# Performance work log

Measured on AMD Instinct MI355X. Metric: run time of the kernel, lower is better.

## Reference

```python
import jax, jax.numpy as jnp
import numpy as np

EPS = 1e-5

def _inst_norm(x):
    # x: (B,C,H,W); torch .var(dim=2) is unbiased (ddof=1) over HW
    B, C, H, W = x.shape
    xf = x.reshape(B, C, H * W)
    mean = xf.mean(axis=2, keepdims=True)
    var = xf.var(axis=2, ddof=1, keepdims=True) + EPS
    return ((xf - mean) / jnp.sqrt(var)).reshape(B, C, H, W)

def _conv1x1(x, w, b):
    # (out,in) weight applied channelwise
    return jnp.einsum('oc,bchw->bohw', w, x) + b[None, :, None, None]

def setup_inputs() -> dict:
    key = jax.random.key(0)
    ks = jax.random.split(key, 10)
    B, C, H, W = 4, 512, 64, 64
    s = 1.0 / np.sqrt(C)
    return {
        'x_fcc': jax.random.normal(ks[0], (B, C, H, W), jnp.float32),
        'x_fss': jax.random.normal(ks[1], (B, C, H, W), jnp.float32),
        'w1': jax.random.normal(ks[2], (C, C), jnp.float32) * s,
        'b1': jax.random.normal(ks[3], (C,), jnp.float32) * 0.01,
        'w2': jax.random.normal(ks[4], (C, C), jnp.float32) * s,
        'b2': jax.random.normal(ks[5], (C,), jnp.float32) * 0.01,
        'w3': jax.random.normal(ks[6], (C, C), jnp.float32) * s,
        'b3': jax.random.normal(ks[7], (C,), jnp.float32) * 0.01,
        'wrs': jax.random.normal(ks[8], (C, C), jnp.float32) * s,
        'brs': jax.random.normal(ks[9], (C,), jnp.float32) * 0.01,
    }

def reference(x_fcc, x_fss, w1, b1, w2, b2, w3, b3, wrs, brs):
    Bc, Cc, Hc, Wc = x_fcc.shape
    Bs, Cs, Hs, Ws = x_fss.shape
    q = _conv1x1(_inst_norm(x_fcc), w1, b1).reshape(Bc, Cc, Hc * Wc)
    k = _conv1x1(_inst_norm(x_fss), w2, b2).reshape(Bs, Cs, Hs * Ws)
    v = _conv1x1(x_fss, w3, b3).reshape(Bc, Cs, Hs * Ws)
    # attention: (B, HWc, HWs), softmax over style positions
    scores = jnp.einsum('bcq,bck->bqk', q, k)
    A = jax.nn.softmax(scores, axis=-1)
    # aggregate style values per content position: (B, C, HWc)
    frs = jnp.einsum('bck,bqk->bcq', v, A).reshape(x_fcc.shape)
    frs = _conv1x1(frs, wrs, brs)
    return frs + x_fcc
```

## Files before the change

### kernel.cpp

```cpp
#include <hip/hip_runtime.h>
#include <hip/hip_bf16.h>


typedef _Float16 f16_t;
typedef _Float16 f16x8 __attribute__((ext_vector_type(8)));
typedef float f32x4 __attribute__((ext_vector_type(4)));

#define C_DIM 512
#define HW_DIM 4096
#define NBATCH 4
#define CHW (512L * 4096L)

__device__ inline f32x4 mfma_f16(f16x8 a, f16x8 b, f32x4 c) {
    return __builtin_amdgcn_mfma_f32_16x16x32_f16(a, b, c, 0, 0, 0);
}

__device__ inline void g2l16(const f16_t* g, f16_t* l) {
    auto gp = (const __attribute__((address_space(1))) uint32_t*)(uintptr_t)g;
    auto lp = (__attribute__((address_space(3))) uint32_t*)(uint32_t)(uintptr_t)l;
    __builtin_amdgcn_global_load_lds(gp, lp, 16, 0, 0);
}

template<int N> __device__ inline void vmwait() {
    static_assert(N == 0 || N == 3 || N == 4 || N == 6, "add vmcnt case");
    if constexpr (N == 0)      asm volatile("s_waitcnt vmcnt(0)" ::: "memory");
    else if constexpr (N == 3) asm volatile("s_waitcnt vmcnt(3)" ::: "memory");
    else if constexpr (N == 4) asm volatile("s_waitcnt vmcnt(4)" ::: "memory");
    else                       asm volatile("s_waitcnt vmcnt(6)" ::: "memory");
}

__global__ __launch_bounds__(256) void stats_kernel(
    const float* __restrict__ xc, const float* __restrict__ xs,
    float* __restrict__ meanc, float* __restrict__ rstdc,
    float* __restrict__ means, float* __restrict__ rstds)
{
    int id = blockIdx.x;
    int bc = id & 2047;
    const float4* x = (const float4*)((id < 2048 ? xc : xs) + (size_t)bc * HW_DIM);
    int tid = threadIdx.x;
    float s = 0.f, ss = 0.f;
#pragma unroll
    for (int i = 0; i < 4; i++) {
        float4 v = x[tid + (i << 8)];
        s += v.x + v.y + v.z + v.w;
        ss += v.x * v.x + v.y * v.y + v.z * v.z + v.w * v.w;
    }
#pragma unroll
    for (int o = 32; o; o >>= 1) { s += __shfl_down(s, o); ss += __shfl_down(ss, o); }
    __shared__ float red[8];
    if ((tid & 63) == 0) { red[(tid >> 6) * 2] = s; red[(tid >> 6) * 2 + 1] = ss; }
    __syncthreads();
    if (tid == 0) {
        s  = red[0] + red[2] + red[4] + red[6];
        ss = red[1] + red[3] + red[5] + red[7];
        float mean = s * (1.0f / 4096.0f);
        float var  = (ss - 4096.0f * mean * mean) * (1.0f / 4095.0f);
        float rstd = rsqrtf(var + 1e-5f);
        if (id < 2048) { meanc[bc] = mean; rstdc[bc] = rstd; }
        else           { means[bc] = mean; rstds[bc] = rstd; }
    }
}

__global__ __launch_bounds__(256) void pack_w4_kernel(
    const float* __restrict__ w0, const float* __restrict__ w1,
    const float* __restrict__ w2, const float* __restrict__ w3,
    f16_t* __restrict__ h0, f16_t* __restrict__ h1,
    f16_t* __restrict__ h2, f16_t* __restrict__ h3,
    const float* __restrict__ bb0, const float* __restrict__ bb1,
    const float* __restrict__ bb2, const float* __restrict__ bb3,
    float* __restrict__ biasws)
{
    int which = blockIdx.y;
    const float* w = which == 0 ? w0 : which == 1 ? w1 : which == 2 ? w2 : w3;
    f16_t* h = which == 0 ? h0 : which == 1 ? h1 : which == 2 ? h2 : h3;
    const float* bs = which == 0 ? bb0 : which == 1 ? bb1 : which == 2 ? bb2 : bb3;
    int i = blockIdx.x * 256 + threadIdx.x;
    h[i] = (f16_t)w[i];
    if (i < C_DIM) biasws[which * C_DIM + i] = bs[i];
}

__global__ __launch_bounds__(256) void pack_T_kernel(
    const float* __restrict__ xc, const float* __restrict__ xs,
    const float* __restrict__ meanc, const float* __restrict__ rstdc,
    const float* __restrict__ means, const float* __restrict__ rstds,
    f16_t* __restrict__ ch, f16_t* __restrict__ sh, f16_t* __restrict__ sraw)
{
    __shared__ float tile[32][33];
    int z = blockIdx.z;
    int b = z & 3, src = z >> 2;
    const float* x    = (src == 0) ? xc : xs;
    const float* mean = (src == 0) ? meanc : means;
    const float* rstd = (src == 0) ? rstdc : rstds;
    f16_t* oh = (src == 0) ? ch : (src == 1) ? sh : sraw;
    bool norm = (src < 2);

    int c0 = blockIdx.y * 32, p0 = blockIdx.x * 32;
    int tp = threadIdx.x & 31, tc8 = threadIdx.x >> 5;
    const float* xb = x + ((size_t)b * C_DIM + c0) * HW_DIM + p0;
#pragma unroll
    for (int it = 0; it < 4; it++) {
        int c = tc8 + it * 8;
        float v = xb[(size_t)c * HW_DIM + tp];
        if (norm) {
            float m = mean[b * C_DIM + c0 + c];
            float r = rstd[b * C_DIM + c0 + c];
            v = (v - m) * r;
        }
        tile[c][tp] = v;
    }
    __syncthreads();
    int wc = threadIdx.x & 31, wp8 = threadIdx.x >> 5;
    f16_t* ohb = oh + ((size_t)b * HW_DIM + p0) * C_DIM + c0;
#pragma unroll
    for (int it = 0; it < 4; it++) {
        int p = wp8 + it * 8;
        ohb[(size_t)p * C_DIM + wc] = (f16_t)tile[wc][p];
    }
}

__global__ __launch_bounds__(256) void softmax_rows(
    const float* __restrict__ S, f16_t* __restrict__ P)
{
    int row = blockIdx.x;
    int tid = threadIdx.x;
    int wave = tid >> 6, lane = tid & 63;
    const float4* sr = (const float4*)(S + (size_t)row * HW_DIM);
    float4 v[4];
    float mx = -3.4e38f;
#pragma unroll
    for (int i = 0; i < 4; i++) {
        v[i] = sr[tid + (i << 8)];
        mx = fmaxf(mx, fmaxf(fmaxf(v[i].x, v[i].y), fmaxf(v[i].z, v[i].w)));
    }
#pragma unroll
    for (int o = 32; o; o >>= 1) mx = fmaxf(mx, __shfl_down(mx, o));
    __shared__ float red[4];
    if (lane == 0) red[wave] = mx;
    __syncthreads();
    mx = fmaxf(fmaxf(red[0], red[1]), fmaxf(red[2], red[3]));
    float sum = 0.f;
#pragma unroll
    for (int i = 0; i < 4; i++) {
        v[i].x = __expf(v[i].x - mx); v[i].y = __expf(v[i].y - mx);
        v[i].z = __expf(v[i].z - mx); v[i].w = __expf(v[i].w - mx);
        sum += v[i].x + v[i].y + v[i].z + v[i].w;
    }
#pragma unroll
    for (int o = 32; o; o >>= 1) sum += __shfl_down(sum, o);
    __syncthreads();
    if (lane == 0) red[wave] = sum;
    __syncthreads();
    sum = red[0] + red[1] + red[2] + red[3];
    float inv = 1.0f / sum;
    uint2* pr = (uint2*)(P + (size_t)row * HW_DIM);
#pragma unroll
    for (int i = 0; i < 4; i++) {
        union { uint2 u; f16_t h[4]; } o;
        o.h[0] = (f16_t)(v[i].x * inv); o.h[1] = (f16_t)(v[i].y * inv);
        o.h[2] = (f16_t)(v[i].z * inv); o.h[3] = (f16_t)(v[i].w * inv);
        pr[tid + (i << 8)] = o.u;
    }
}

__global__ __launch_bounds__(256) void reduce4_kernel(
    const float* __restrict__ part, f16_t* __restrict__ out)
{
    size_t i = (size_t)blockIdx.x * 256 + threadIdx.x;
    const float4* p0 = (const float4*)part;
    const float4* p1 = (const float4*)(part + CHW);
    const float4* p2 = (const float4*)(part + 2 * CHW);
    const float4* p3 = (const float4*)(part + 3 * CHW);
    float4 a = p0[i], b = p1[i], c = p2[i], d = p3[i];
    union { uint2 u; f16_t h[4]; } o;
    o.h[0] = (f16_t)(a.x + b.x + c.x + d.x);
    o.h[1] = (f16_t)(a.y + b.y + c.y + d.y);
    o.h[2] = (f16_t)(a.z + b.z + c.z + d.z);
    o.h[3] = (f16_t)(a.w + b.w + c.w + d.w);
    ((uint2*)out)[i] = o.u;
}

template<int WM, int WN, int EPI, bool QK, int KT, int CHX, int CHY>
__global__ __launch_bounds__(256) void gemm_nt(
    const f16_t* __restrict__ Ah, const f16_t* __restrict__ Bh,
    void* __restrict__ Cout0,
    const float* __restrict__ bias, const float* __restrict__ resid,
    int lda, int ldc,
    long sAz, long sBz, long sCz, long sRz, long sAw, long sBw, long sCw)
{
    constexpr int BM = 2 * WM * 16;
    constexpr int BN = 2 * WN * 16;
    constexpr int BK = 32;
    constexpr int NIT = KT / BK;
    constexpr int BUFSZ = (BM + BN) * BK;
    constexpr int AOPS = BM / 64;
    constexpr int BOPS = BN / 64;
    constexpr int OPS  = AOPS + BOPS;
    __shared__ __align__(16) f16_t smem[3 * BUFSZ];

    int bx, by, bz;
    if constexpr (CHX > 0) {
        const int nbx = gridDim.x, nby = gridDim.y, nbz = gridDim.z;
        const int lin = (blockIdx.z * nby + blockIdx.y) * nbx + blockIdx.x;
        const int nwg = nbx * nby * nbz;
        const int cpx = nwg >> 3;
        const int logical = (lin & 7) * cpx + (lin >> 3);
        constexpr int CHB = CHX * CHY;
        const int chunk  = logical / CHB;
        const int within = logical % CHB;
        const int cx = within % CHX, cy = within / CHX;
        const int chunks_x = nbx / CHX;
        const int chx = chunk % chunks_x;
        int t = chunk / chunks_x;
        const int chunks_y = nby / CHY;
        const int chy = t % chunks_y;
        bz = t / chunks_y;
        bx = chx * CHX + cx;
        by = chy * CHY + cy;
    } else {
        bx = blockIdx.x; by = blockIdx.y; bz = blockIdx.z;
    }

    const int tid  = threadIdx.x;
    const int wave = tid >> 6, lane = tid & 63;
    const int wm = (wave >> 1) * (WM * 16);
    const int wn = (wave & 1) * (WN * 16);
    const int fr = lane & 15;
    const int fk = (lane >> 4) * 8;
    const int srow = lane >> 2;
    const int scol = (lane & 3) * 8;

    const long mBlock = (long)by * BM;
    const long nBlock = (long)bx * BN;
    const int zz = bz;
    const int z   = QK ? (zz & 3) : zz;
    const int sel = QK ? (zz >> 2) : 0;
    const f16_t* Az = Ah + (size_t)z * sAz + (size_t)sel * sAw;
    const f16_t* Bz = Bh + (size_t)z * sBz + (size_t)sel * sBw;
    const float* biasp = bias ? (bias + (QK ? sel * C_DIM : 0)) : nullptr;

    const f16_t* gA = Az + (size_t)(mBlock + srow) * lda + scol;
    const f16_t* gB = Bz + (size_t)(nBlock + srow) * lda + scol;

    const f16_t* srcA[AOPS]; int dstA[AOPS];
    const f16_t* srcB[BOPS]; int dstB[BOPS];
#pragma unroll
    for (int i = 0; i < AOPS; i++) {
        int seg = i * 4 + wave;
        srcA[i] = gA + (size_t)seg * 16 * lda;
        dstA[i] = seg * 512;
    }
#pragma unroll
    for (int i = 0; i < BOPS; i++) {
        int seg = i * 4 + wave;
        srcB[i] = gB + (size_t)seg * 16 * lda;
        dstB[i] = BM * BK + seg * 512;
    }

    auto stage = [&](int t) {
        f16_t* dst = smem + (t % 3) * BUFSZ;
        const int k0 = t * BK;
#pragma unroll
        for (int i = 0; i < AOPS; i++) g2l16(srcA[i] + k0, dst + dstA[i]);
#pragma unroll
        for (int i = 0; i < BOPS; i++) g2l16(srcB[i] + k0, dst + dstB[i]);
    };

    f32x4 acc[WM][WN];
#pragma unroll
    for (int i = 0; i < WM; i++)
#pragma unroll
        for (int j = 0; j < WN; j++)
            acc[i][j] = (f32x4){0.f, 0.f, 0.f, 0.f};

    stage(0);
    stage(1);
    vmwait<OPS>();
    __builtin_amdgcn_s_barrier();
    __builtin_amdgcn_sched_barrier(0);

#pragma unroll
    for (int t = 0; t < NIT; ++t) {
        if (t + 2 < NIT) {
            stage(t + 2);
            __builtin_amdgcn_sched_barrier(0);
        }
        const f16_t* sA = smem + (t % 3) * BUFSZ;
        const f16_t* sB = sA + BM * BK;
        f16x8 af[WM], bf[WN];
#pragma unroll
        for (int i = 0; i < WM; i++)
            af[i] = *reinterpret_cast<const f16x8*>(sA + (wm + i * 16 + fr) * BK + fk);
#pragma unroll
        for (int j = 0; j < WN; j++)
            bf[j] = *reinterpret_cast<const f16x8*>(sB + (wn + j * 16 + fr) * BK + fk);
        __builtin_amdgcn_s_setprio(1);
#pragma unroll
        for (int i = 0; i < WM; i++)
#pragma unroll
            for (int j = 0; j < WN; j++)
                acc[i][j] = mfma_f16(af[i], bf[j], acc[i][j]);
        __builtin_amdgcn_s_setprio(0);

        if (t + 2 < NIT)      vmwait<OPS>();
        else if (t + 1 < NIT) vmwait<0>();
        if (t + 1 < NIT) {
            __builtin_amdgcn_s_barrier();
            __builtin_amdgcn_sched_barrier(0);
        }
    }

    const int col  = lane & 15;
    const int rowq = (lane >> 4) * 4;
    const size_t cbase = (size_t)z * sCz + (size_t)sel * sCw;
#pragma unroll
    for (int i = 0; i < WM; i++) {
        const long mb = mBlock + wm + i * 16 + rowq;
        float bv[4];
#pragma unroll
        for (int r = 0; r < 4; r++) bv[r] = biasp ? biasp[mb + r] : 0.0f;
#pragma unroll
        for (int j = 0; j < WN; j++) {
            const long n = nBlock + wn + j * 16 + col;
            float v[4];
#pragma unroll
            for (int r = 0; r < 4; r++) v[r] = acc[i][j][r] + bv[r];
            if constexpr (EPI == 0) {
                float* O = (float*)Cout0 + cbase;
                const float* R = resid ? (resid + (size_t)z * sRz) : nullptr;
#pragma unroll
                for (int r = 0; r < 4; r++) {
                    size_t off = (size_t)(mb + r) * ldc + n;
                    O[off] = v[r] + (R ? R[off] : 0.0f);
                }
            } else if constexpr (EPI == 1) {
                f16_t* O = (f16_t*)Cout0 + cbase;
#pragma unroll
                for (int r = 0; r < 4; r++) O[(size_t)(mb + r) * ldc + n] = (f16_t)v[r];
            } else if constexpr (EPI == 3) {
                alignas(8) f16_t h[4];
#pragma unroll
                for (int r = 0; r < 4; r++) h[r] = (f16_t)v[r];
                size_t offo = cbase + (size_t)n * ldc + mb;
                *reinterpret_cast<uint2*>((f16_t*)Cout0 + offo) = *reinterpret_cast<uint2*>(h);
            } else {
                alignas(16) float h[4];
#pragma unroll
                for (int r = 0; r < 4; r++) h[r] = v[r];
                size_t offo = cbase + (size_t)n * ldc + mb;
                *reinterpret_cast<float4*>((float*)Cout0 + offo) = *reinterpret_cast<float4*>(h);
            }
        }
    }
}

extern "C" void kernel_launch(void* const* d_in, const int* in_sizes, int n_in,
                              void* d_out, int out_size, void* d_ws, size_t ws_size,
                              hipStream_t stream)
{
    const float* x_fcc = (const float*)d_in[0];
    const float* x_fss = (const float*)d_in[1];
    const float* w1 = (const float*)d_in[2];
    const float* b1 = (const float*)d_in[3];
    const float* w2 = (const float*)d_in[4];
    const float* b2 = (const float*)d_in[5];
    const float* w3 = (const float*)d_in[6];
    const float* b3 = (const float*)d_in[7];
    const float* wrs = (const float*)d_in[8];
    const float* brs = (const float*)d_in[9];
    float* out = (float*)d_out;
    (void)n_in; (void)in_sizes; (void)out_size; (void)ws_size;

    char* base = (char*)d_ws;
    size_t off = 0;
    auto take = [&](size_t bytes) -> char* {
        char* p = base + off;
        off += (bytes + 255) & ~(size_t)255;
        return p;
    };
    const size_t WB = (size_t)C_DIM * C_DIM * sizeof(f16_t);
    const size_t TB = (size_t)NBATCH * CHW * sizeof(f16_t);
    const long  TBe = NBATCH * CHW;

    float* meanc = (float*)take(2048 * 4);
    float* rstdc = (float*)take(2048 * 4);
    float* means = (float*)take(2048 * 4);
    float* rstds = (float*)take(2048 * 4);
    float* biasws = (float*)take(4 * C_DIM * 4);
    f16_t* w1h = (f16_t*)take(WB);
    f16_t* w2h = (f16_t*)take(WB);
    f16_t* w3h = (f16_t*)take(WB);
    f16_t* wrh = (f16_t*)take(WB);
    f16_t* qT = (f16_t*)take(TB);
    f16_t* kT = (f16_t*)take(TB);
    f16_t* vh   = (f16_t*)take(TB);
    f16_t* frsT = (f16_t*)take(TB);
    char* packb = take(8 * TB);
    f16_t* xcT  = (f16_t*)(packb);
    f16_t* xsT  = (f16_t*)(packb + TB);
    f16_t* xsrT = (f16_t*)(packb + 2 * TB);
    float* Smat = (float*)(packb);
    f16_t* Pmat = (f16_t*)(packb + 4 * TB);
    float* Part = (float*)(packb + 6 * TB);

    dim3 blk(256);

    stats_kernel<<<dim3(4096), blk, 0, stream>>>(x_fcc, x_fss, meanc, rstdc, means, rstds);
    pack_w4_kernel<<<dim3(1024, 4), blk, 0, stream>>>(
        w1, w2, w3, wrs, w1h, w2h, w3h, wrh, b1, b2, b3, brs, biasws);
    pack_T_kernel<<<dim3(128, 16, 12), blk, 0, stream>>>(
        x_fcc, x_fss, meanc, rstdc, means, rstds, xcT, xsT, xsrT);
    gemm_nt<4, 4, 3, true, C_DIM, 16, 4><<<dim3(32, 4, 8), blk, 0, stream>>>(
        w1h, xcT, qT, biasws, nullptr, C_DIM, C_DIM,
        0L, CHW, CHW, 0L, (long)C_DIM * C_DIM, TBe, TBe);
    gemm_nt<4, 4, 1, false, C_DIM, 16, 4><<<dim3(32, 4, 4), blk, 0, stream>>>(
        w3h, xsrT, vh, biasws + 2 * C_DIM, nullptr, C_DIM, HW_DIM,
        0L, CHW, CHW, 0L, 0L, 0L, 0L);
    for (int b = 0; b < NBATCH; b++) {
        gemm_nt<4, 4, 0, false, C_DIM, 8, 8><<<dim3(32, 32, 1), blk, 0, stream>>>(
            qT + (size_t)b * CHW, kT + (size_t)b * CHW,
            Smat, nullptr, nullptr, C_DIM, HW_DIM,
            0L, 0L, 0L, 0L, 0L, 0L, 0L);
        softmax_rows<<<dim3(4096), blk, 0, stream>>>(Smat, Pmat);
        gemm_nt<2, 4, 4, false, 1024, 8, 8><<<dim3(32, 8, 4), blk, 0, stream>>>(
            vh + (size_t)b * CHW, Pmat,
            Part, nullptr, nullptr, HW_DIM, C_DIM,
            1024L, 1024L, CHW, 0L, 0L, 0L, 0L);
        reduce4_kernel<<<dim3(CHW / 1024), blk, 0, stream>>>(
            Part, frsT + (size_t)b * CHW);
    }
    gemm_nt<4, 4, 0, false, C_DIM, 16, 4><<<dim3(32, 4, 4), blk, 0, stream>>>(
        wrh, frsT, out, biasws + 3 * C_DIM, x_fcc, C_DIM, HW_DIM,
        0L, CHW, CHW, CHW, 0L, 0L, 0L);
}
```

Baseline: 599.3 us.

## Add 256x128 swizzled-LDS GEMM kernel for QK, scores and PV with split-K 8

```diff
diff --git a/kernel.cpp b/kernel.cpp
--- a/kernel.cpp
+++ b/kernel.cpp
@@ -27,6 +27,11 @@
     else if constexpr (N == 3) asm volatile("s_waitcnt vmcnt(3)" ::: "memory");
     else if constexpr (N == 4) asm volatile("s_waitcnt vmcnt(4)" ::: "memory");
     else                       asm volatile("s_waitcnt vmcnt(6)" ::: "memory");
+}
+
+__device__ inline void barrier_mem() {
+    asm volatile("s_barrier" ::: "memory");
+    __builtin_amdgcn_sched_barrier(0);
 }
 
 __global__ __launch_bounds__(256) void stats_kernel(
@@ -162,21 +167,177 @@
     }
 }
 
-__global__ __launch_bounds__(256) void reduce4_kernel(
+__global__ __launch_bounds__(256) void reduce8_kernel(
     const float* __restrict__ part, f16_t* __restrict__ out)
 {
     size_t i = (size_t)blockIdx.x * 256 + threadIdx.x;
-    const float4* p0 = (const float4*)part;
-    const float4* p1 = (const float4*)(part + CHW);
-    const float4* p2 = (const float4*)(part + 2 * CHW);
-    const float4* p3 = (const float4*)(part + 3 * CHW);
-    float4 a = p0[i], b = p1[i], c = p2[i], d = p3[i];
+    float4 s = ((const float4*)part)[i];
+#pragma unroll
+    for (int p = 1; p < 8; p++) {
+        float4 v = ((const float4*)(part + (size_t)p * CHW))[i];
+        s.x += v.x; s.y += v.y; s.z += v.z; s.w += v.w;
+    }
     union { uint2 u; f16_t h[4]; } o;
-    o.h[0] = (f16_t)(a.x + b.x + c.x + d.x);
-    o.h[1] = (f16_t)(a.y + b.y + c.y + d.y);
-    o.h[2] = (f16_t)(a.z + b.z + c.z + d.z);
-    o.h[3] = (f16_t)(a.w + b.w + c.w + d.w);
+    o.h[0] = (f16_t)s.x; o.h[1] = (f16_t)s.y;
+    o.h[2] = (f16_t)s.z; o.h[3] = (f16_t)s.w;
     ((uint2*)out)[i] = o.u;
+}
+
+template<int EPI, bool QK, int CHX, int CHY>
+__global__ __launch_bounds__(512, 2) void gemm256(
+    const f16_t* __restrict__ Ah, const f16_t* __restrict__ Bh,
+    void* __restrict__ Cout0, const float* __restrict__ bias,
+    int lda, int ldc,
+    long sAz, long sBz, long sCz, long sAw, long sBw, long sCw)
+{
+    constexpr int NT = 8;
+    constexpr int AE = 256 * 64;
+    constexpr int BE = 128 * 64;
+    constexpr int BUFE = AE + BE;
+    __shared__ __align__(16) f16_t smem[3 * BUFE];
+
+    int bx, by, bz;
+    {
+        const int nbx = gridDim.x, nby = gridDim.y, nbz = gridDim.z;
+        const int lin = ((int)blockIdx.z * nby + blockIdx.y) * nbx + blockIdx.x;
+        const int nwg = nbx * nby * nbz;
+        const int cpx = nwg >> 3;
+        const int logical = (lin & 7) * cpx + (lin >> 3);
+        constexpr int CHB = CHX * CHY;
+        const int chunk  = logical / CHB;
+        const int within = logical % CHB;
+        const int cx = within % CHX, cy = within / CHX;
+        const int chunks_x = nbx / CHX;
+        const int chx = chunk % chunks_x;
+        int tt = chunk / chunks_x;
+        const int chunks_y = nby / CHY;
+        bz = tt / chunks_y;
+        by = (tt % chunks_y) * CHY + cy;
+        bx = chx * CHX + cx;
+    }
+
+    const int tid  = threadIdx.x;
+    const int wave = tid >> 6, lane = tid & 63;
+    const int wm = (wave >> 2) * 128;
+    const int wn = (wave & 3) * 32;
+    const int fr = lane & 15;
+    const int g16 = lane >> 4;
+    const int key = fr & 7;
+
+    const int z   = QK ? (bz & 3) : bz;
+    const int sel = QK ? (bz >> 2) : 0;
+    const f16_t* Az = Ah + (size_t)z * sAz + (size_t)sel * sAw;
+    const f16_t* Bz = Bh + (size_t)z * sBz + (size_t)sel * sBw;
+    const float* biasp = bias ? (bias + (QK ? sel * C_DIM : 0)) : nullptr;
+    const long mBlock = (long)by * 256;
+    const long nBlock = (long)bx * 128;
+
+    const int srow8 = lane >> 3;
+    const int gsrc  = ((lane & 7) ^ srow8) * 8;
+    const f16_t* aSrc[4]; const f16_t* bSrc[2];
+    int aDst[4], bDst[2];
+#pragma unroll
+    for (int q = 0; q < 4; q++) {
+        int j = 4 * wave + q;
+        aSrc[q] = Az + (size_t)(mBlock + 8 * j + srow8) * lda + gsrc;
+        aDst[q] = j * 512;
+    }
+#pragma unroll
+    for (int q = 0; q < 2; q++) {
+        int j = 2 * wave + q;
+        bSrc[q] = Bz + (size_t)(nBlock + 8 * j + srow8) * lda + gsrc;
+        bDst[q] = AE + j * 512;
+    }
+
+    auto stageA = [&](int t) {
+        f16_t* dst = smem + (t % 3) * BUFE;
+        const int k0 = t * 64;
+#pragma unroll
+        for (int q = 0; q < 4; q++) g2l16(aSrc[q] + k0, dst + aDst[q]);
+    };
+    auto stageB = [&](int t) {
+        f16_t* dst = smem + (t % 3) * BUFE;
+        const int k0 = t * 64;
+#pragma unroll
+        for (int q = 0; q < 2; q++) g2l16(bSrc[q] + k0, dst + bDst[q]);
+    };
+
+    f32x4 acc[8][2];
+#pragma unroll
+    for (int i = 0; i < 8; i++)
+#pragma unroll
+        for (int j = 0; j < 2; j++) acc[i][j] = (f32x4){0.f, 0.f, 0.f, 0.f};
+
+    stageA(0); stageB(0); stageA(1); stageB(1);
+    vmwait<6>();
+    barrier_mem();
+
+#pragma unroll
+    for (int t = 0; t < NT; ++t) {
+        const f16_t* buf = smem + (t % 3) * BUFE;
+#pragma unroll
+        for (int ks = 0; ks < 2; ++ks) {
+            f16x8 a[8], b[2];
+            const int gr = ((ks * 4 + g16) ^ key) * 8;
+#pragma unroll
+            for (int j2 = 0; j2 < 2; j2++)
+                b[j2] = *reinterpret_cast<const f16x8*>(
+                    buf + AE + (wn + j2 * 16 + fr) * 64 + gr);
+#pragma unroll
+            for (int mi = 0; mi < 8; mi++)
+                a[mi] = *reinterpret_cast<const f16x8*>(
+                    buf + (wm + mi * 16 + fr) * 64 + gr);
+            if (t + 2 < NT) { if (ks == 0) stageA(t + 2); else stageB(t + 2); }
+            if (ks == 1) {
+                if (t + 2 < NT)      vmwait<6>();
+                else if (t + 1 < NT) vmwait<0>();
+            }
+            barrier_mem();
+            __builtin_amdgcn_s_setprio(1);
+#pragma unroll
+            for (int mi = 0; mi < 8; mi++)
+#pragma unroll
+                for (int j2 = 0; j2 < 2; j2++)
+                    acc[mi][j2] = mfma_f16(a[mi], b[j2], acc[mi][j2]);
+            __builtin_amdgcn_s_setprio(0);
+            barrier_mem();
+        }
+    }
+
+    const int col  = lane & 15;
+    const int rowq = (lane >> 4) * 4;
+    const size_t cbase = (size_t)z * sCz + (size_t)sel * sCw;
+#pragma unroll
+    for (int mi = 0; mi < 8; mi++) {
+        const long mb = mBlock + wm + mi * 16 + rowq;
+        float bv[4];
+#pragma unroll
+        for (int r = 0; r < 4; r++) bv[r] = biasp ? biasp[mb + r] : 0.0f;
+#pragma unroll
+        for (int j2 = 0; j2 < 2; j2++) {
+            const long n = nBlock + wn + j2 * 16 + col;
+            float v[4];
+#pragma unroll
+            for (int r = 0; r < 4; r++) v[r] = acc[mi][j2][r] + bv[r];
+            if constexpr (EPI == 0) {
+                float* O = (float*)Cout0 + cbase;
+#pragma unroll
+                for (int r = 0; r < 4; r++) O[(size_t)(mb + r) * ldc + n] = v[r];
+            } else if constexpr (EPI == 3) {
+                alignas(8) f16_t h[4];
+#pragma unroll
+                for (int r = 0; r < 4; r++) h[r] = (f16_t)v[r];
+                *reinterpret_cast<uint2*>((f16_t*)Cout0 + cbase + (size_t)n * ldc + mb)
+                    = *reinterpret_cast<uint2*>(h);
+            } else {
+                alignas(16) float h[4];
+#pragma unroll
+                for (int r = 0; r < 4; r++) h[r] = v[r];
+                *reinterpret_cast<float4*>((float*)Cout0 + cbase + (size_t)n * ldc + mb)
+                    = *reinterpret_cast<float4*>(h);
+            }
+        }
+    }
 }
 
 template<int WM, int WN, int EPI, bool QK, int KT, int CHX, int CHY>
@@ -280,10 +441,7 @@
 
 #pragma unroll
     for (int t = 0; t < NIT; ++t) {
-        if (t + 2 < NIT) {
-            stage(t + 2);
-            __builtin_amdgcn_sched_barrier(0);
-        }
+        if (t + 2 < NIT) stage(t + 2);
         const f16_t* sA = smem + (t % 3) * BUFSZ;
         const f16_t* sB = sA + BM * BK;
         f16x8 af[WM], bf[WN];
@@ -293,13 +451,11 @@
 #pragma unroll
         for (int j = 0; j < WN; j++)
             bf[j] = *reinterpret_cast<const f16x8*>(sB + (wn + j * 16 + fr) * BK + fk);
-        __builtin_amdgcn_s_setprio(1);
 #pragma unroll
         for (int i = 0; i < WM; i++)
 #pragma unroll
             for (int j = 0; j < WN; j++)
                 acc[i][j] = mfma_f16(af[i], bf[j], acc[i][j]);
-        __builtin_amdgcn_s_setprio(0);
 
         if (t + 2 < NIT)      vmwait<OPS>();
         else if (t + 1 < NIT) vmwait<0>();
@@ -400,32 +556,33 @@
     f16_t* xsrT = (f16_t*)(packb + 2 * TB);
     float* Smat = (float*)(packb);
     f16_t* Pmat = (f16_t*)(packb + 4 * TB);
-    float* Part = (float*)(packb + 6 * TB);
+    float* Part = (float*)(packb);
 
     dim3 blk(256);
+    dim3 blk5(512);
 
     stats_kernel<<<dim3(4096), blk, 0, stream>>>(x_fcc, x_fss, meanc, rstdc, means, rstds);
     pack_w4_kernel<<<dim3(1024, 4), blk, 0, stream>>>(
         w1, w2, w3, wrs, w1h, w2h, w3h, wrh, b1, b2, b3, brs, biasws);
     pack_T_kernel<<<dim3(128, 16, 12), blk, 0, stream>>>(
         x_fcc, x_fss, meanc, rstdc, means, rstds, xcT, xsT, xsrT);
-    gemm_nt<4, 4, 3, true, C_DIM, 16, 4><<<dim3(32, 4, 8), blk, 0, stream>>>(
-        w1h, xcT, qT, biasws, nullptr, C_DIM, C_DIM,
-        0L, CHW, CHW, 0L, (long)C_DIM * C_DIM, TBe, TBe);
+    gemm256<3, true, 8, 2><<<dim3(32, 2, 8), blk5, 0, stream>>>(
+        w1h, xcT, qT, biasws, C_DIM, C_DIM,
+        0L, CHW, CHW, (long)C_DIM * C_DIM, TBe, TBe);
     gemm_nt<4, 4, 1, false, C_DIM, 16, 4><<<dim3(32, 4, 4), blk, 0, stream>>>(
         w3h, xsrT, vh, biasws + 2 * C_DIM, nullptr, C_DIM, HW_DIM,
         0L, CHW, CHW, 0L, 0L, 0L, 0L);
     for (int b = 0; b < NBATCH; b++) {
-        gemm_nt<4, 4, 0, false, C_DIM, 8, 8><<<dim3(32, 32, 1), blk, 0, stream>>>(
+        gemm256<0, false, 8, 4><<<dim3(32, 16, 1), blk5, 0, stream>>>(
             qT + (size_t)b * CHW, kT + (size_t)b * CHW,
-            Smat, nullptr, nullptr, C_DIM, HW_DIM,
-            0L, 0L, 0L, 0L, 0L, 0L, 0L);
+            Smat, nullptr, C_DIM, HW_DIM,
+            0L, 0L, 0L, 0L, 0L, 0L);
         softmax_rows<<<dim3(4096), blk, 0, stream>>>(Smat, Pmat);
-        gemm_nt<2, 4, 4, false, 1024, 8, 8><<<dim3(32, 8, 4), blk, 0, stream>>>(
+        gemm256<4, false, 8, 2><<<dim3(32, 2, 8), blk5, 0, stream>>>(
             vh + (size_t)b * CHW, Pmat,
-            Part, nullptr, nullptr, HW_DIM, C_DIM,
-            1024L, 1024L, CHW, 0L, 0L, 0L, 0L);
-        reduce4_kernel<<<dim3(CHW / 1024), blk, 0, stream>>>(
+            Part, nullptr, HW_DIM, C_DIM,
+            512L, 512L, (long)CHW, 0L, 0L, 0L);
+        reduce8_kernel<<<dim3(CHW / 1024), blk, 0, stream>>>(
             Part, frsT + (size_t)b * CHW);
     }
     gemm_nt<4, 4, 0, false, C_DIM, 16, 4><<<dim3(32, 4, 4), blk, 0, stream>>>(
```

New measurement: 557.9 us. 6.9% less time.

## Replace GEMM with 256x128 tiled 512-thread kernel using swizzled LDS and BK=64

Applied to the files above, without the earlier changes.

```diff
diff --git a/kernel.cpp b/kernel.cpp
--- a/kernel.cpp
+++ b/kernel.cpp
@@ -22,11 +22,14 @@
 }
 
 template<int N> __device__ inline void vmwait() {
-    static_assert(N == 0 || N == 3 || N == 4 || N == 6, "add vmcnt case");
-    if constexpr (N == 0)      asm volatile("s_waitcnt vmcnt(0)" ::: "memory");
-    else if constexpr (N == 3) asm volatile("s_waitcnt vmcnt(3)" ::: "memory");
-    else if constexpr (N == 4) asm volatile("s_waitcnt vmcnt(4)" ::: "memory");
-    else                       asm volatile("s_waitcnt vmcnt(6)" ::: "memory");
+    static_assert(N == 0 || N == 6, "add vmcnt case");
+    if constexpr (N == 0) asm volatile("s_waitcnt vmcnt(0)" ::: "memory");
+    else                  asm volatile("s_waitcnt vmcnt(6)" ::: "memory");
+}
+
+__device__ inline void barrier_mem() {
+    asm volatile("s_barrier" ::: "memory");
+    __builtin_amdgcn_sched_barrier(0);
 }
 
 __global__ __launch_bounds__(256) void stats_kernel(
@@ -91,8 +94,6 @@
     const float* x    = (src == 0) ? xc : xs;
     const float* mean = (src == 0) ? meanc : means;
     const float* rstd = (src == 0) ? rstdc : rstds;
-    f16_t* oh = (src == 0) ? ch : (src == 1) ? sh : sraw;
-    bool norm = (src < 2);
 
     int c0 = blockIdx.y * 32, p0 = blockIdx.x * 32;
     int tp = threadIdx.x & 31, tc8 = threadIdx.x >> 5;
@@ -100,21 +101,21 @@
 #pragma unroll
     for (int it = 0; it < 4; it++) {
         int c = tc8 + it * 8;
-        float v = xb[(size_t)c * HW_DIM + tp];
-        if (norm) {
-            float m = mean[b * C_DIM + c0 + c];
-            float r = rstd[b * C_DIM + c0 + c];
-            v = (v - m) * r;
-        }
-        tile[c][tp] = v;
+        tile[c][tp] = xb[(size_t)c * HW_DIM + tp];
     }
     __syncthreads();
     int wc = threadIdx.x & 31, wp8 = threadIdx.x >> 5;
-    f16_t* ohb = oh + ((size_t)b * HW_DIM + p0) * C_DIM + c0;
+    float m = mean[b * C_DIM + c0 + wc];
+    float r = rstd[b * C_DIM + c0 + wc];
+    size_t obase = ((size_t)b * HW_DIM + p0) * C_DIM + c0;
+    f16_t* ohb = ((src == 0) ? ch : sh) + obase;
+    f16_t* srb = sraw + obase;
 #pragma unroll
     for (int it = 0; it < 4; it++) {
         int p = wp8 + it * 8;
-        ohb[(size_t)p * C_DIM + wc] = (f16_t)tile[wc][p];
+        float v = tile[wc][p];
+        ohb[(size_t)p * C_DIM + wc] = (f16_t)((v - m) * r);
+        if (src == 1) srb[(size_t)p * C_DIM + wc] = (f16_t)v;
     }
 }
 
@@ -179,28 +180,23 @@
     ((uint2*)out)[i] = o.u;
 }
 
-template<int WM, int WN, int EPI, bool QK, int KT, int CHX, int CHY>
-__global__ __launch_bounds__(256) void gemm_nt(
+template<int EPI, bool QK, int NT, int CHX, int CHY>
+__global__ __launch_bounds__(512, 2) void gemm256(
     const f16_t* __restrict__ Ah, const f16_t* __restrict__ Bh,
-    void* __restrict__ Cout0,
-    const float* __restrict__ bias, const float* __restrict__ resid,
+    void* __restrict__ Cout0, const float* __restrict__ bias,
+    const float* __restrict__ resid,
     int lda, int ldc,
     long sAz, long sBz, long sCz, long sRz, long sAw, long sBw, long sCw)
 {
-    constexpr int BM = 2 * WM * 16;
-    constexpr int BN = 2 * WN * 16;
-    constexpr int BK = 32;
-    constexpr int NIT = KT / BK;
-    constexpr int BUFSZ = (BM + BN) * BK;
-    constexpr int AOPS = BM / 64;
-    constexpr int BOPS = BN / 64;
-    constexpr int OPS  = AOPS + BOPS;
-    __shared__ __align__(16) f16_t smem[3 * BUFSZ];
+    constexpr int AE = 256 * 64;
+    constexpr int BE = 128 * 64;
+    constexpr int BUFE = AE + BE;
+    __shared__ __align__(16) f16_t smem[3 * BUFE];
 
     int bx, by, bz;
-    if constexpr (CHX > 0) {
+    {
         const int nbx = gridDim.x, nby = gridDim.y, nbz = gridDim.z;
-        const int lin = (blockIdx.z * nby + blockIdx.y) * nbx + blockIdx.x;
+        const int lin = ((int)blockIdx.z * nby + blockIdx.y) * nbx + blockIdx.x;
         const int nwg = nbx * nby * nbz;
         const int cpx = nwg >> 3;
         const int logical = (lin & 7) * cpx + (lin >> 3);
@@ -210,102 +206,98 @@
         const int cx = within % CHX, cy = within / CHX;
         const int chunks_x = nbx / CHX;
         const int chx = chunk % chunks_x;
-        int t = chunk / chunks_x;
+        int tt = chunk / chunks_x;
         const int chunks_y = nby / CHY;
-        const int chy = t % chunks_y;
-        bz = t / chunks_y;
+        bz = tt / chunks_y;
+        by = (tt % chunks_y) * CHY + cy;
         bx = chx * CHX + cx;
-        by = chy * CHY + cy;
-    } else {
-        bx = blockIdx.x; by = blockIdx.y; bz = blockIdx.z;
     }
 
     const int tid  = threadIdx.x;
     const int wave = tid >> 6, lane = tid & 63;
-    const int wm = (wave >> 1) * (WM * 16);
-    const int wn = (wave & 1) * (WN * 16);
+    const int wm = (wave >> 2) * 128;
+    const int wn = (wave & 3) * 32;
     const int fr = lane & 15;
-    const int fk = (lane >> 4) * 8;
-    const int srow = lane >> 2;
-    const int scol = (lane & 3) * 8;
-
-    const long mBlock = (long)by * BM;
-    const long nBlock = (long)bx * BN;
-    const int zz = bz;
-    const int z   = QK ? (zz & 3) : zz;
-    const int sel = QK ? (zz >> 2) : 0;
+    const int g16 = lane >> 4;
+    const int key = fr & 7;
+
+    const int z   = QK ? (bz & 3) : bz;
+    const int sel = QK ? (bz >> 2) : 0;
     const f16_t* Az = Ah + (size_t)z * sAz + (size_t)sel * sAw;
     const f16_t* Bz = Bh + (size_t)z * sBz + (size_t)sel * sBw;
     const float* biasp = bias ? (bias + (QK ? sel * C_DIM : 0)) : nullptr;
-
-    const f16_t* gA = Az + (size_t)(mBlock + srow) * lda + scol;
-    const f16_t* gB = Bz + (size_t)(nBlock + srow) * lda + scol;
-
-    const f16_t* srcA[AOPS]; int dstA[AOPS];
-    const f16_t* srcB[BOPS]; int dstB[BOPS];
-#pragma unroll
-    for (int i = 0; i < AOPS; i++) {
-        int seg = i * 4 + wave;
-        srcA[i] = gA + (size_t)seg * 16 * lda;
-        dstA[i] = seg * 512;
-    }
-#pragma unroll
-    for (int i = 0; i < BOPS; i++) {
-        int seg = i * 4 + wave;
-        srcB[i] = gB + (size_t)seg * 16 * lda;
-        dstB[i] = BM * BK + seg * 512;
-    }
-
-    auto stage = [&](int t) {
-        f16_t* dst = smem + (t % 3) * BUFSZ;
-        const int k0 = t * BK;
-#pragma unroll
-        for (int i = 0; i < AOPS; i++) g2l16(srcA[i] + k0, dst + dstA[i]);
-#pragma unroll
-        for (int i = 0; i < BOPS; i++) g2l16(srcB[i] + k0, dst + dstB[i]);
+    const long mBlock = (long)by * 256;
+    const long nBlock = (long)bx * 128;
+
+    const int srow8 = lane >> 3;
+    const int gsrc  = ((lane & 7) ^ srow8) * 8;
+    const f16_t* aSrc[4]; const f16_t* bSrc[2];
+    int aDst[4], bDst[2];
+#pragma unroll
+    for (int q = 0; q < 4; q++) {
+        int j = 4 * wave + q;
+        aSrc[q] = Az + (size_t)(mBlock + 8 * j + srow8) * lda + gsrc;
+        aDst[q] = j * 512;
+    }
+#pragma unroll
+    for (int q = 0; q < 2; q++) {
+        int j = 2 * wave + q;
+        bSrc[q] = Bz + (size_t)(nBlock + 8 * j + srow8) * lda + gsrc;
+        bDst[q] = AE + j * 512;
+    }
+
+    auto stageA = [&](int t) {
+        f16_t* dst = smem + (t % 3) * BUFE;
+        const int k0 = t * 64;
+#pragma unroll
+        for (int q = 0; q < 4; q++) g2l16(aSrc[q] + k0, dst + aDst[q]);
     };
-
-    f32x4 acc[WM][WN];
-#pragma unroll
-    for (int i = 0; i < WM; i++)
-#pragma unroll
-        for (int j = 0; j < WN; j++)
-            acc[i][j] = (f32x4){0.f, 0.f, 0.f, 0.f};
-
-    stage(0);
-    stage(1);
-    vmwait<OPS>();
-    __builtin_amdgcn_s_barrier();
-    __builtin_amdgcn_sched_barrier(0);
-
-#pragma unroll
-    for (int t = 0; t < NIT; ++t) {
-        if (t + 2 < NIT) {
-            stage(t + 2);
-            __builtin_amdgcn_sched_barrier(0);
-        }
-        const f16_t* sA = smem + (t % 3) * BUFSZ;
-        const f16_t* sB = sA + BM * BK;
-        f16x8 af[WM], bf[WN];
-#pragma unroll
-        for (int i = 0; i < WM; i++)
-            af[i] = *reinterpret_cast<const f16x8*>(sA + (wm + i * 16 + fr) * BK + fk);
-#pragma unroll
-        for (int j = 0; j < WN; j++)
-            bf[j] = *reinterpret_cast<const f16x8*>(sB + (wn + j * 16 + fr) * BK + fk);
-        __builtin_amdgcn_s_setprio(1);
-#pragma unroll
-        for (int i = 0; i < WM; i++)
-#pragma unroll
-            for (int j = 0; j < WN; j++)
-                acc[i][j] = mfma_f16(af[i], bf[j], acc[i][j]);
-        __builtin_amdgcn_s_setprio(0);
-
-        if (t + 2 < NIT)      vmwait<OPS>();
-        else if (t + 1 < NIT) vmwait<0>();
-        if (t + 1 < NIT) {
-            __builtin_amdgcn_s_barrier();
-            __builtin_amdgcn_sched_barrier(0);
+    auto stageB = [&](int t) {
+        f16_t* dst = smem + (t % 3) * BUFE;
+        const int k0 = t * 64;
+#pragma unroll
+        for (int q = 0; q < 2; q++) g2l16(bSrc[q] + k0, dst + bDst[q]);
+    };
+
+    f32x4 acc[8][2];
+#pragma unroll
+    for (int i = 0; i < 8; i++)
+#pragma unroll
+        for (int j = 0; j < 2; j++) acc[i][j] = (f32x4){0.f, 0.f, 0.f, 0.f};
+
+    stageA(0); stageB(0); stageA(1); stageB(1);
+    vmwait<6>();
+    barrier_mem();
+
+#pragma unroll
+    for (int t = 0; t < NT; ++t) {
+        const f16_t* buf = smem + (t % 3) * BUFE;
+#pragma unroll
+        for (int ks = 0; ks < 2; ++ks) {
+            f16x8 a[8], b[2];
+            const int gr = ((ks * 4 + g16) ^ key) * 8;
+#pragma unroll
+            for (int j2 = 0; j2 < 2; j2++)
+                b[j2] = *reinterpret_cast<const f16x8*>(
+                    buf + AE + (wn + j2 * 16 + fr) * 64 + gr);
+#pragma unroll
+            for (int mi = 0; mi < 8; mi++)
+                a[mi] = *reinterpret_cast<const f16x8*>(
+                    buf + (wm + mi * 16 + fr) * 64 + gr);
+            if (t + 2 < NT) { if (ks == 0) stageA(t + 2); else stageB(t + 2); }
+            if (ks == 1) {
+                if (t + 2 < NT)      vmwait<6>();
+                else if (t + 1 < NT) vmwait<0>();
+            }
+            barrier_mem();
+            __builtin_amdgcn_s_setprio(1);
+#pragma unroll
+            for (int mi = 0; mi < 8; mi++)
+#pragma unroll
+                for (int j2 = 0; j2 < 2; j2++)
+                    acc[mi][j2] = mfma_f16(a[mi], b[j2], acc[mi][j2]);
+            __builtin_amdgcn_s_setprio(0);
+            barrier_mem();
         }
     }
 
@@ -313,17 +305,17 @@
     const int rowq = (lane >> 4) * 4;
     const size_t cbase = (size_t)z * sCz + (size_t)sel * sCw;
 #pragma unroll
-    for (int i = 0; i < WM; i++) {
-        const long mb = mBlock + wm + i * 16 + rowq;
+    for (int mi = 0; mi < 8; mi++) {
+        const long mb = mBlock + wm + mi * 16 + rowq;
         float bv[4];
 #pragma unroll
         for (int r = 0; r < 4; r++) bv[r] = biasp ? biasp[mb + r] : 0.0f;
 #pragma unroll
-        for (int j = 0; j < WN; j++) {
-            const long n = nBlock + wn + j * 16 + col;
+        for (int j2 = 0; j2 < 2; j2++) {
+            const long n = nBlock + wn + j2 * 16 + col;
             float v[4];
 #pragma unroll
-            for (int r = 0; r < 4; r++) v[r] = acc[i][j][r] + bv[r];
+            for (int r = 0; r < 4; r++) v[r] = acc[mi][j2][r] + bv[r];
             if constexpr (EPI == 0) {
                 float* O = (float*)Cout0 + cbase;
                 const float* R = resid ? (resid + (size_t)z * sRz) : nullptr;
@@ -340,14 +332,14 @@
                 alignas(8) f16_t h[4];
 #pragma unroll
                 for (int r = 0; r < 4; r++) h[r] = (f16_t)v[r];
-                size_t offo = cbase + (size_t)n * ldc + mb;
-                *reinterpret_cast<uint2*>((f16_t*)Cout0 + offo) = *reinterpret_cast<uint2*>(h);
+                *reinterpret_cast<uint2*>((f16_t*)Cout0 + cbase + (size_t)n * ldc + mb)
+                    = *reinterpret_cast<uint2*>(h);
             } else {
                 alignas(16) float h[4];
 #pragma unroll
                 for (int r = 0; r < 4; r++) h[r] = v[r];
-                size_t offo = cbase + (size_t)n * ldc + mb;
-                *reinterpret_cast<float4*>((float*)Cout0 + offo) = *reinterpret_cast<float4*>(h);
+                *reinterpret_cast<float4*>((float*)Cout0 + cbase + (size_t)n * ldc + mb)
+                    = *reinterpret_cast<float4*>(h);
             }
         }
     }
@@ -403,32 +395,33 @@
     float* Part = (float*)(packb + 6 * TB);
 
     dim3 blk(256);
+    dim3 blk5(512);
 
     stats_kernel<<<dim3(4096), blk, 0, stream>>>(x_fcc, x_fss, meanc, rstdc, means, rstds);
     pack_w4_kernel<<<dim3(1024, 4), blk, 0, stream>>>(
         w1, w2, w3, wrs, w1h, w2h, w3h, wrh, b1, b2, b3, brs, biasws);
-    pack_T_kernel<<<dim3(128, 16, 12), blk, 0, stream>>>(
+    pack_T_kernel<<<dim3(128, 16, 8), blk, 0, stream>>>(
         x_fcc, x_fss, meanc, rstdc, means, rstds, xcT, xsT, xsrT);
-    gemm_nt<4, 4, 3, true, C_DIM, 16, 4><<<dim3(32, 4, 8), blk, 0, stream>>>(
+    gemm256<3, true, 8, 8, 2><<<dim3(32, 2, 8), blk5, 0, stream>>>(
         w1h, xcT, qT, biasws, nullptr, C_DIM, C_DIM,
         0L, CHW, CHW, 0L, (long)C_DIM * C_DIM, TBe, TBe);
-    gemm_nt<4, 4, 1, false, C_DIM, 16, 4><<<dim3(32, 4, 4), blk, 0, stream>>>(
+    gemm256<1, false, 8, 8, 2><<<dim3(32, 2, 4), blk5, 0, stream>>>(
         w3h, xsrT, vh, biasws + 2 * C_DIM, nullptr, C_DIM, HW_DIM,
         0L, CHW, CHW, 0L, 0L, 0L, 0L);
     for (int b = 0; b < NBATCH; b++) {
-        gemm_nt<4, 4, 0, false, C_DIM, 8, 8><<<dim3(32, 32, 1), blk, 0, stream>>>(
+        gemm256<0, false, 8, 8, 4><<<dim3(32, 16, 1), blk5, 0, stream>>>(
             qT + (size_t)b * CHW, kT + (size_t)b * CHW,
             Smat, nullptr, nullptr, C_DIM, HW_DIM,
             0L, 0L, 0L, 0L, 0L, 0L, 0L);
         softmax_rows<<<dim3(4096), blk, 0, stream>>>(Smat, Pmat);
-        gemm_nt<2, 4, 4, false, 1024, 8, 8><<<dim3(32, 8, 4), blk, 0, stream>>>(
+        gemm256<4, false, 16, 8, 2><<<dim3(32, 2, 4), blk5, 0, stream>>>(
             vh + (size_t)b * CHW, Pmat,
             Part, nullptr, nullptr, HW_DIM, C_DIM,
             1024L, 1024L, CHW, 0L, 0L, 0L, 0L);
         reduce4_kernel<<<dim3(CHW / 1024), blk, 0, stream>>>(
             Part, frsT + (size_t)b * CHW);
     }
-    gemm_nt<4, 4, 0, false, C_DIM, 16, 4><<<dim3(32, 4, 4), blk, 0, stream>>>(
+    gemm256<0, false, 8, 8, 2><<<dim3(32, 2, 4), blk5, 0, stream>>>(
         wrh, frsT, out, biasws + 3 * C_DIM, x_fcc, C_DIM, HW_DIM,
         0L, CHW, CHW, CHW, 0L, 0L, 0L);
 }
```

Measured after the change: 533.4 us. -11.0%, faster.
